# Optimization experiments

Hardware: AMD Instinct MI355X
Metric: run time of the kernel (lower is better)

## Reference

```python
import math
import jax, jax.numpy as jnp
import numpy as np

OLEN = 512
RATIO = 0.5
DROP_P = 0.2


def _gat(x, src, dst, W, a_s, a_d, b):
    """PyG GATConv (heads=1, concat=True, add_self_loops=True, neg_slope=0.2)."""
    n = x.shape[0]
    loops = jnp.arange(n, dtype=src.dtype)
    s = jnp.concatenate([src, loops])  # [E+N] source nodes
    d = jnp.concatenate([dst, loops])  # [E+N] destination nodes
    h = x @ W                           # [N, H]
    alpha_s = h @ a_s                   # [N]
    alpha_d = h @ a_d                   # [N]
    e = jax.nn.leaky_relu(alpha_s[s] + alpha_d[d], 0.2)  # [E+N]
    # segment softmax over destination neighborhoods
    m = jax.ops.segment_max(e, d, num_segments=n)
    ee = jnp.exp(e - m[d])
    denom = jax.ops.segment_sum(ee, d, num_segments=n)
    alpha = ee / denom[d]
    out = jax.ops.segment_sum(alpha[:, None] * h[s], d, num_segments=n)
    return out + b


def _forward(x, src, dst, W1, a_src1, a_dst1, b1, W2, a_src2, a_dst2, b2,
             W3, a_src3, a_dst3, b3, W_rel, W_root, b_pool):
    N, E = x.shape[0], src.shape[0]
    key = jax.random.key(42)
    h = x
    for i, (W, a_s, a_d, b) in enumerate([(W1, a_src1, a_dst1, b1),
                                          (W2, a_src2, a_dst2, b2),
                                          (W3, a_src3, a_dst3, b3)]):
        h = jax.nn.relu(_gat(h, src, dst, W, a_s, a_d, b))
        keep = jax.random.bernoulli(jax.random.fold_in(key, i), 1.0 - DROP_P, h.shape)
        h = jnp.where(keep, h / (1.0 - DROP_P), 0.0)  # F.dropout(training=True)

    # SAGPooling(GraphConv score, ratio=0.5, tanh) repeated until n <= 512.
    # Node counts are static per iteration (k = ceil(0.5*n)); edge arrays keep
    # fixed size E with a validity mask (edges dropped when an endpoint is pooled away).
    cur_src, cur_dst = src, dst
    emask = jnp.ones((E,), dtype=h.dtype)
    n = N
    while True:
        agg = jax.ops.segment_sum(h[cur_src] * emask[:, None], cur_dst, num_segments=n)
        score = (agg @ W_rel + h @ W_root + b_pool)[:, 0]  # GraphConv(d->1), aggr='add'
        score = jnp.tanh(score)
        k = math.ceil(RATIO * n)
        top_vals, perm = jax.lax.top_k(score, k)
        h = h[perm] * top_vals[:, None]
        inv = jnp.full((n,), -1, dtype=cur_src.dtype).at[perm].set(
            jnp.arange(k, dtype=cur_src.dtype))
        ns, nd = inv[cur_src], inv[cur_dst]
        valid = (ns >= 0) & (nd >= 0)
        emask = emask * valid.astype(emask.dtype)
        cur_src = jnp.where(valid, ns, 0)
        cur_dst = jnp.where(valid, nd, 0)
        n = k
        if n <= OLEN:
            break

    out = jnp.zeros((OLEN, h.shape[1]), h.dtype).at[:n].set(h)
    return out


def setup_inputs() -> dict:
    key = jax.random.key(0)
    ks = jax.random.split(key, 20)
    N, E, IDIM, HDIM = 50000, 800000, 128, 200
    inp = {
        "x": jax.random.normal(ks[0], (N, IDIM), jnp.float32),
        "src": jax.random.randint(ks[1], (E,), 0, N, jnp.int32),
        "dst": jax.random.randint(ks[2], (E,), 0, N, jnp.int32),
    }
    def w(k, shape, fan_in):
        return jax.random.normal(k, shape, jnp.float32) / np.sqrt(fan_in).astype(np.float32)
    inp["W1"] = w(ks[3], (IDIM, HDIM), IDIM)
    inp["a_src1"] = w(ks[4], (HDIM,), HDIM)
    inp["a_dst1"] = w(ks[5], (HDIM,), HDIM)
    inp["b1"] = jnp.zeros((HDIM,), jnp.float32)
    inp["W2"] = w(ks[6], (HDIM, HDIM), HDIM)
    inp["a_src2"] = w(ks[7], (HDIM,), HDIM)
    inp["a_dst2"] = w(ks[8], (HDIM,), HDIM)
    inp["b2"] = jnp.zeros((HDIM,), jnp.float32)
    inp["W3"] = w(ks[9], (HDIM, HDIM), HDIM)
    inp["a_src3"] = w(ks[10], (HDIM,), HDIM)
    inp["a_dst3"] = w(ks[11], (HDIM,), HDIM)
    inp["b3"] = jnp.zeros((HDIM,), jnp.float32)
    inp["W_rel"] = w(ks[12], (HDIM, 1), HDIM)
    inp["W_root"] = w(ks[13], (HDIM, 1), HDIM)
    inp["b_pool"] = jnp.zeros((1,), jnp.float32)
    return inp


def reference(x, src, dst, W1, a_src1, a_dst1, b1, W2, a_src2, a_dst2, b2,
              W3, a_src3, a_dst3, b3, W_rel, W_root, b_pool):
    return _forward(x, src, dst, W1, a_src1, a_dst1, b1, W2, a_src2, a_dst2, b2,
                    W3, a_src3, a_dst3, b3, W_rel, W_root, b_pool)
```

## Files before the change

kernel.cpp:

```cpp
#include <hip/hip_runtime.h>
#include <cstdint>
#include <cstddef>


__host__ __device__ inline void tf_round(uint32_t &x0, uint32_t &x1, int r) {
  x0 += x1;
  x1 = (x1 << r) | (x1 >> (32 - r));
  x1 ^= x0;
}

__host__ __device__ inline void threefry2x32(uint32_t k0, uint32_t k1,
                                             uint32_t &x0, uint32_t &x1) {
  uint32_t ks2 = k0 ^ k1 ^ 0x1BD11BDAu;
  x0 += k0; x1 += k1;
  tf_round(x0, x1, 13); tf_round(x0, x1, 15); tf_round(x0, x1, 26); tf_round(x0, x1, 6);
  x0 += k1; x1 += ks2 + 1u;
  tf_round(x0, x1, 17); tf_round(x0, x1, 29); tf_round(x0, x1, 16); tf_round(x0, x1, 24);
  x0 += ks2; x1 += k0 + 2u;
  tf_round(x0, x1, 13); tf_round(x0, x1, 15); tf_round(x0, x1, 26); tf_round(x0, x1, 6);
  x0 += k0; x1 += k1 + 3u;
  tf_round(x0, x1, 17); tf_round(x0, x1, 29); tf_round(x0, x1, 16); tf_round(x0, x1, 24);
  x0 += k1; x1 += ks2 + 4u;
  tf_round(x0, x1, 13); tf_round(x0, x1, 15); tf_round(x0, x1, 26); tf_round(x0, x1, 6);
  x0 += ks2; x1 += k0 + 5u;
}

__global__ __launch_bounds__(256) void gemm200_k(
    const float* __restrict__ A, const float* __restrict__ B,
    float* __restrict__ C, int M, int K) {
  __shared__ float As[128 * 9];
  __shared__ __align__(16) float Bs[8][208];
  int tid = threadIdx.x;
  int m0 = blockIdx.x * 128;
  int r = tid >> 2;
  int colBase = (tid & 3) * 52;
  int nq = (colBase == 156) ? 11 : 13;
  float acc0[52], acc1[52];
#pragma unroll
  for (int q = 0; q < 52; q++) { acc0[q] = 0.f; acc1[q] = 0.f; }

  int arow = tid >> 1;
  int ac = (tid & 1) * 4;
  int gmA = m0 + arow;
  const float* Aptr = A + (size_t)gmA * K + ac;
  int bk0 = tid / 50, bc0 = (tid - bk0 * 50) * 4;
  int t2 = tid + 256;
  int bk1 = t2 / 50, bc1 = (t2 - bk1 * 50) * 4;
  bool hasB1 = (t2 < 400);

  float4 va = make_float4(0.f, 0.f, 0.f, 0.f);
  if (gmA < M) va = *(const float4*)(Aptr);
  float4 vb0 = *(const float4*)(B + (size_t)bk0 * 200 + bc0);
  float4 vb1 = make_float4(0.f, 0.f, 0.f, 0.f);
  if (hasB1) vb1 = *(const float4*)(B + (size_t)bk1 * 200 + bc1);

  for (int k0 = 0; k0 < K; k0 += 8) {
    As[arow * 9 + ac + 0] = va.x;
    As[arow * 9 + ac + 1] = va.y;
    As[arow * 9 + ac + 2] = va.z;
    As[arow * 9 + ac + 3] = va.w;
    *(float4*)(&Bs[bk0][bc0]) = vb0;
    if (hasB1) *(float4*)(&Bs[bk1][bc1]) = vb1;
    __syncthreads();
    int kn = k0 + 8;
    if (kn < K) {
      if (gmA < M) va = *(const float4*)(Aptr + kn);
      vb0 = *(const float4*)(B + (size_t)(kn + bk0) * 200 + bc0);
      if (hasB1) vb1 = *(const float4*)(B + (size_t)(kn + bk1) * 200 + bc1);
    }
#pragma unroll
    for (int kk = 0; kk < 8; kk++) {
      float a0 = As[r * 9 + kk];
      float a1 = As[(r + 64) * 9 + kk];
#pragma unroll
      for (int q = 0; q < 13; q++) {
        float4 b = *(const float4*)(&Bs[kk][colBase + 4 * q]);
        acc0[4 * q + 0] += a0 * b.x; acc0[4 * q + 1] += a0 * b.y;
        acc0[4 * q + 2] += a0 * b.z; acc0[4 * q + 3] += a0 * b.w;
        acc1[4 * q + 0] += a1 * b.x; acc1[4 * q + 1] += a1 * b.y;
        acc1[4 * q + 2] += a1 * b.z; acc1[4 * q + 3] += a1 * b.w;
      }
    }
    __syncthreads();
  }
  int gm0 = m0 + r, gm1 = m0 + r + 64;
#pragma unroll
  for (int q = 0; q < 13; q++) {
    if (q < nq) {
      int col = colBase + 4 * q;
      float4 v0 = make_float4(acc0[4 * q + 0], acc0[4 * q + 1],
                              acc0[4 * q + 2], acc0[4 * q + 3]);
      float4 v1 = make_float4(acc1[4 * q + 0], acc1[4 * q + 1],
                              acc1[4 * q + 2], acc1[4 * q + 3]);
      if (gm0 < M) *(float4*)(C + (size_t)gm0 * 200 + col) = v0;
      if (gm1 < M) *(float4*)(C + (size_t)gm1 * 200 + col) = v1;
    }
  }
}

__global__ __launch_bounds__(256) void dual_dot_k(
    const float* __restrict__ H, const float* __restrict__ v1,
    const float* __restrict__ v2, float* __restrict__ o1,
    float* __restrict__ o2, int n) {
  int wave = blockIdx.x * 4 + (threadIdx.x >> 6);
  int lane = threadIdx.x & 63;
  if (wave >= n) return;
  const float* row = H + (size_t)wave * 200;
  float s1 = 0.f, s2 = 0.f;
  for (int d = lane; d < 200; d += 64) {
    float h = row[d];
    s1 += h * v1[d];
    s2 += h * v2[d];
  }
  for (int off = 32; off; off >>= 1) {
    s1 += __shfl_down(s1, off);
    s2 += __shfl_down(s2, off);
  }
  if (lane == 0) { o1[wave] = s1; o2[wave] = s2; }
}

__global__ __launch_bounds__(256) void indeg_k(const int* __restrict__ dst,
                                               int* __restrict__ cnt, int E) {
  int e = blockIdx.x * 256 + threadIdx.x;
  if (e < E) atomicAdd(&cnt[dst[e]], 1);
}

__global__ __launch_bounds__(256) void scan_k(const int* __restrict__ cnt,
                                              int* __restrict__ rowptr, int N) {
  __shared__ int psum[256];
  int t = threadIdx.x;
  int CH = (N + 255) / 256;
  int beg = t * CH, end = min(beg + CH, N);
  if (beg > N) { beg = N; }
  int s = 0;
  for (int i = beg; i < end; i++) s += cnt[i];
  psum[t] = s;
  __syncthreads();
  if (t == 0) {
    int run = 0;
    for (int i = 0; i < 256; i++) { int v = psum[i]; psum[i] = run; run += v; }
  }
  __syncthreads();
  int run = psum[t];
  for (int i = beg; i < end; i++) { rowptr[i] = run; run += cnt[i]; }
  if (end == N && beg <= N) rowptr[N] = run;
}

__global__ __launch_bounds__(256) void cpyint_k(const int* __restrict__ a,
                                                int* __restrict__ b, int n) {
  int i = blockIdx.x * 256 + threadIdx.x;
  if (i < n) b[i] = a[i];
}

__global__ __launch_bounds__(256) void place_k(const int* __restrict__ dst,
                                               int* __restrict__ curs,
                                               int* __restrict__ csr, int E) {
  int e = blockIdx.x * 256 + threadIdx.x;
  if (e >= E) return;
  int pos = atomicAdd(&curs[dst[e]], 1);
  csr[pos] = e;
}

__global__ __launch_bounds__(256) void sortrow_k(const int* __restrict__ rowptr,
                                                 int* __restrict__ csr, int N) {
  int d = blockIdx.x * 256 + threadIdx.x;
  if (d >= N) return;
  int b = rowptr[d], e2 = rowptr[d + 1];
  for (int i = b + 1; i < e2; i++) {
    int v = csr[i];
    int j = i - 1;
    while (j >= b && csr[j] > v) { csr[j + 1] = csr[j]; j--; }
    csr[j + 1] = v;
  }
}

__device__ inline float dec_ord(unsigned enc) {
  unsigned b = (enc & 0x80000000u) ? (enc ^ 0x80000000u) : ~enc;
  return __uint_as_float(b);
}

__global__ __launch_bounds__(256) void edge_max_k(
    const int* __restrict__ src, const int* __restrict__ dst,
    const float* __restrict__ as_, const float* __restrict__ ad_,
    unsigned* __restrict__ menc, int E, int N) {
  int j = blockIdx.x * 256 + threadIdx.x;
  if (j >= E + N) return;
  int s, d;
  if (j < E) { s = src[j]; d = dst[j]; } else { s = j - E; d = s; }
  float v = as_[s] + ad_[d];
  float ev = (v >= 0.f) ? v : 0.2f * v;
  unsigned b = __float_as_uint(ev);
  unsigned enc = (b & 0x80000000u) ? ~b : (b | 0x80000000u);
  atomicMax(&menc[d], enc);
}

__global__ __launch_bounds__(256) void eeden_k(
    const int* __restrict__ rowptr, const int* __restrict__ csr,
    const int* __restrict__ src, const float* __restrict__ as_,
    const float* __restrict__ ad_, const unsigned* __restrict__ menc,
    int2* __restrict__ pk, float* __restrict__ eeS, float* __restrict__ den,
    int N) {
  int d = blockIdx.x * 256 + threadIdx.x;
  if (d >= N) return;
  float m = dec_ord(menc[d]);
  float adv = ad_[d];
  int b = rowptr[d], e2 = rowptr[d + 1];
  float s = 0.f;
  for (int i = b; i < e2; i++) {
    int e = csr[i];
    int sv = src[e];
    float v = as_[sv] + adv;
    float ev = (v >= 0.f) ? v : 0.2f * v;
    float ee = expf(ev - m);
    pk[i] = make_int2(sv, __float_as_int(ee));
    s = __fadd_rn(s, ee);
  }
  float vS = as_[d] + adv;
  float evS = (vS >= 0.f) ? vS : 0.2f * vS;
  float eS = expf(evS - m);
  eeS[d] = eS;
  s = __fadd_rn(s, eS);
  den[d] = s;
}

#define GLD(s) (*(const float4*)(Hl + (size_t)(s) * 200))
#define ACC(W_, H_)                                    \
  acc.x = __fadd_rn(acc.x, __fmul_rn((W_), (H_).x));   \
  acc.y = __fadd_rn(acc.y, __fmul_rn((W_), (H_).y));   \
  acc.z = __fadd_rn(acc.z, __fmul_rn((W_), (H_).z));   \
  acc.w = __fadd_rn(acc.w, __fmul_rn((W_), (H_).w));

__global__ __launch_bounds__(256) void gat_out_k(
    const int* __restrict__ rowptr, const int2* __restrict__ pk,
    const float* __restrict__ eeS, const float* __restrict__ den,
    const float* __restrict__ HW, float* __restrict__ OUT, int N) {
  int node = blockIdx.x * 4 + (threadIdx.x >> 6);
  int lane = threadIdx.x & 63;
  if (node >= N || lane >= 50) return;
  int b = rowptr[node];
  int deg = rowptr[node + 1] - b;
  int cnt = deg + 1;
  float dn = den[node];
  const float* __restrict__ Hl = HW + 4 * lane;

  auto fS = [&](int t, int &s, float &w) {
    if (t < deg) {
      int2 p = pk[b + t];
      s = p.x;
      w = __fdiv_rn(__int_as_float(p.y), dn);
    } else if (t == deg) {
      s = node;
      w = __fdiv_rn(eeS[node], dn);
    } else {
      s = node;
      w = 0.f;
    }
  };

  int sa, sb, sc, sd, se, sf, sn;
  float w0, w1, w2, w3, w4, w5, wn;
  fS(0, sa, w0); fS(1, sb, w1); fS(2, sc, w2); fS(3, sd, w3);
  float4 h0 = GLD(sa), h1 = GLD(sb), h2 = GLD(sc), h3 = GLD(sd);
  fS(4, se, w4);
  fS(5, sf, w5);

  float4 acc = make_float4(0.f, 0.f, 0.f, 0.f);
  for (int t = 0; t < cnt; t++) {
    float4 h4 = GLD(se);
    fS(t + 6, sn, wn);
    ACC(w0, h0);
    h0 = h1; h1 = h2; h2 = h3; h3 = h4;
    w0 = w1; w1 = w2; w2 = w3; w3 = w4; w4 = w5; w5 = wn;
    se = sf; sf = sn;
  }
  *(float4*)(OUT + (size_t)node * 200 + 4 * lane) = acc;
}

__global__ __launch_bounds__(256) void epi_k(float* __restrict__ H,
                                             const float* __restrict__ bias,
                                             uint32_t k0, uint32_t k1, int total) {
  int t = blockIdx.x * 256 + threadIdx.x;
  if (t >= total) return;
  uint32_t x0 = 0u, x1 = (uint32_t)t;
  threefry2x32(k0, k1, x0, x1);
  uint32_t bits = x0 ^ x1;
  float u = __uint_as_float((bits >> 9) | 0x3f800000u) - 1.0f;
  int col = t % 200;
  float v = H[t] + bias[col];
  v = fmaxf(v, 0.f);
  H[t] = (u < 0.8f) ? (v / 0.8f) : 0.f;
}

__global__ __launch_bounds__(256) void einit_k(
    const int* __restrict__ src, const int* __restrict__ dst,
    int* __restrict__ cs, int* __restrict__ cd, int* __restrict__ orig,
    int E, int N) {
  int e = blockIdx.x * 256 + threadIdx.x;
  if (e < E) { cs[e] = src[e]; cd[e] = dst[e]; }
  if (e < N) orig[e] = e;
}

__global__ __launch_bounds__(256) void pool_agg_k(
    const int* __restrict__ rowptr, const int* __restrict__ csr,
    const int* __restrict__ csrc, const int* __restrict__ orig,
    const float* __restrict__ H, const float* __restrict__ wrel,
    const float* __restrict__ wroot, const float* __restrict__ bp,
    float* __restrict__ score, int n) {
  __shared__ float sagg[4][200];
  int wv = threadIdx.x >> 6;
  int node = blockIdx.x * 4 + wv;
  int lane = threadIdx.x & 63;
  if (node >= n) return;
  int o = orig[node];
  int b = rowptr[o];
  int deg = rowptr[o + 1] - b;

  if (lane < 50) {
    const float* __restrict__ Hl = H + 4 * lane;
    auto fS = [&](int t, int &s, float &w) {
      if (t < deg) {
        int e = csr[b + t];
        int sv = csrc[e];
        s = (sv >= 0) ? sv : 0;
        w = (sv >= 0) ? 1.f : 0.f;
      } else {
        s = 0;
        w = 0.f;
      }
    };

    int sa, sb, sc, sd, se, sf, sn;
    float w0, w1, w2, w3, w4, w5, wn;
    fS(0, sa, w0); fS(1, sb, w1); fS(2, sc, w2); fS(3, sd, w3);
    float4 h0 = GLD(sa), h1 = GLD(sb), h2 = GLD(sc), h3 = GLD(sd);
    fS(4, se, w4);
    fS(5, sf, w5);

    float4 acc = make_float4(0.f, 0.f, 0.f, 0.f);
    for (int t = 0; t < deg; t++) {
      float4 h4 = GLD(se);
      fS(t + 6, sn, wn);
      ACC(w0, h0);
      h0 = h1; h1 = h2; h2 = h3; h3 = h4;
      w0 = w1; w1 = w2; w2 = w3; w3 = w4; w4 = w5; w5 = wn;
      se = sf; sf = sn;
    }
    sagg[wv][4 * lane + 0] = acc.x;
    sagg[wv][4 * lane + 1] = acc.y;
    sagg[wv][4 * lane + 2] = acc.z;
    sagg[wv][4 * lane + 3] = acc.w;
  }
  __threadfence_block();

  const float* arow = sagg[wv];
  const float* hrow = H + (size_t)node * 200;
  float s1 = 0.f, s2 = 0.f;
  for (int d = lane; d < 200; d += 64) {
    s1 += arow[d] * wrel[d];
    s2 += hrow[d] * wroot[d];
  }
  for (int off = 32; off; off >>= 1) {
    s1 += __shfl_down(s1, off);
    s2 += __shfl_down(s2, off);
  }
  if (lane == 0) score[node] = tanhf((s1 + s2) + bp[0]);
}
#undef GLD
#undef ACC


__global__ __launch_bounds__(256) void rhenc_k(const float* __restrict__ score,
                                               unsigned* __restrict__ keyA,
                                               int* __restrict__ payA,
                                               int* __restrict__ counts,
                                               int n, int NB) {
  __shared__ int hist[256];
  hist[threadIdx.x] = 0;
  __syncthreads();
  int i = blockIdx.x * 256 + threadIdx.x;
  if (i < n) {
    unsigned b = __float_as_uint(score[i]);
    if (b == 0x80000000u) b = 0u;
    unsigned enc = (b & 0x80000000u) ? ~b : (b | 0x80000000u);
    unsigned key = ~enc;
    keyA[i] = key;
    payA[i] = i;
    atomicAdd(&hist[key & 255u], 1);
  }
  __syncthreads();
  counts[threadIdx.x * NB + blockIdx.x] = hist[threadIdx.x];
}

__global__ __launch_bounds__(256) void rscan_k(int* __restrict__ counts,
                                               int* __restrict__ base, int NB) {
  __shared__ int tot[256];
  int t = threadIdx.x;
  int s = 0;
  for (int b = 0; b < NB; b++) s += counts[t * NB + b];
  tot[t] = s;
  __syncthreads();
  if (t == 0) {
    int run = 0;
    for (int i = 0; i < 256; i++) { int v = tot[i]; tot[i] = run; run += v; }
  }
  __syncthreads();
  int run = tot[t];
  for (int b = 0; b < NB; b++) {
    int c = counts[t * NB + b];
    base[t * NB + b] = run;
    run += c;
    counts[t * NB + b] = 0;
  }
}

__global__ __launch_bounds__(256) void rscatter_k(
    const unsigned* __restrict__ keyIn, const int* __restrict__ payIn,
    const int* __restrict__ base, unsigned* __restrict__ keyOut,
    int* __restrict__ payOut, int* __restrict__ countsNext,
    int n, int NB, int shift) {
  __shared__ int dig[256];
  int t = threadIdx.x;
  int i = blockIdx.x * 256 + t;
  unsigned k = 0u;
  int p = 0, d = -1;
  if (i < n) {
    k = keyIn[i];
    p = payIn[i];
    d = (int)((k >> shift) & 255u);
  }
  dig[t] = d;
  __syncthreads();
  if (i < n) {
    int local = 0;
    for (int j = 0; j < t; j++) local += (dig[j] == d) ? 1 : 0;
    int pos = base[d * NB + blockIdx.x] + local;
    keyOut[pos] = k;
    payOut[pos] = p;
    int nd = (int)((k >> (shift + 8)) & 255u);
    atomicAdd(&countsNext[nd * NB + (pos >> 8)], 1);
  }
}

__global__ __launch_bounds__(256) void rscatterF_k(
    const unsigned* __restrict__ keyIn, const int* __restrict__ payIn,
    const int* __restrict__ base, const int* __restrict__ oin,
    int* __restrict__ oout, int* __restrict__ perm, int* __restrict__ inv,
    int n, int NB, int k) {
  __shared__ int dig[256];
  int t = threadIdx.x;
  int i = blockIdx.x * 256 + t;
  int p = 0, d = -1;
  if (i < n) {
    p = payIn[i];
    d = (int)((keyIn[i] >> 24) & 255u);
  }
  dig[t] = d;
  __syncthreads();
  if (i < n) {
    int local = 0;
    for (int j = 0; j < t; j++) local += (dig[j] == d) ? 1 : 0;
    int pos = base[d * NB + blockIdx.x] + local;
    if (pos < k) { perm[pos] = p; inv[p] = pos; oout[pos] = oin[p]; }
    else inv[p] = -1;
  }
}

__global__ __launch_bounds__(256) void gather_k(
    const float* __restrict__ H, const int* __restrict__ perm,
    const float* __restrict__ score, float* __restrict__ Ho, int k) {
  int r = blockIdx.x;
  int d = threadIdx.x;
  int p = perm[r];
  float s = score[p];
  if (d < 200) Ho[(size_t)r * 200 + d] = __fmul_rn(H[(size_t)p * 200 + d], s);
}

__global__ __launch_bounds__(256) void remap_k(int* __restrict__ cs,
                                               int* __restrict__ cd,
                                               const int* __restrict__ inv, int E) {
  int e = blockIdx.x * 256 + threadIdx.x;
  if (e >= E) return;
  int a = cs[e];
  if (a < 0) return;
  int na = inv[a], nb = inv[cd[e]];
  bool valid = (na >= 0) && (nb >= 0);
  cs[e] = valid ? na : -1;
  cd[e] = valid ? nb : -1;
}

__global__ __launch_bounds__(256) void out_copy_k(const float* __restrict__ h,
                                                  float* __restrict__ out, int cnt) {
  int t = blockIdx.x * 256 + threadIdx.x;
  if (t < cnt) out[t] = h[t];
}

extern "C" void kernel_launch(void* const* d_in, const int* in_sizes, int n_in,
                              void* d_out, int out_size, void* d_ws, size_t ws_size,
                              hipStream_t stream) {
  const int ID = 128, HD = 200;
  const int N = in_sizes[0] / ID;
  const int E = in_sizes[1];
  const int ET = E + N;
  const int total = N * HD;

  const float* x = (const float*)d_in[0];
  const int* src = (const int*)d_in[1];
  const int* dst = (const int*)d_in[2];
  const float* W[3]   = {(const float*)d_in[3], (const float*)d_in[7], (const float*)d_in[11]};
  const float* asv[3] = {(const float*)d_in[4], (const float*)d_in[8], (const float*)d_in[12]};
  const float* adv[3] = {(const float*)d_in[5], (const float*)d_in[9], (const float*)d_in[13]};
  const float* bv[3]  = {(const float*)d_in[6], (const float*)d_in[10], (const float*)d_in[14]};
  const float* Wrel  = (const float*)d_in[15];
  const float* Wroot = (const float*)d_in[16];
  const float* bpool = (const float*)d_in[17];

  char* ws = (char*)d_ws;
  float*    bufA  = (float*)(ws + 0);
  float*    bufB  = (float*)(ws + 40000000);
  float*    as_   = (float*)(ws + 80000000);
  float*    ad_   = (float*)(ws + 80200000);
  float*    ee_   = (float*)(ws + 80400000);
  unsigned* menc  = (unsigned*)(ws + 83800000);
  float*    den   = (float*)(ws + 84000000);
  float*    score = (float*)(ws + 84200000);
  int*      rank_ = (int*)(ws + 84400000);
  int*      perm_ = (int*)(ws + 84600000);
  int*      inv_  = (int*)(ws + 84800000);
  int*      origA = (int*)(ws + 85000000);
  int*      origB = (int*)(ws + 85200000);
  int*      rowptr= (int*)(ws + 85400000);
  int*      curs  = (int*)(ws + 85650000);
  int*      csr   = (int*)(ws + 85850000);
  int*      csrc  = (int*)(ws + 89050000);
  int*      cdst  = (int*)(ws + 92250000);

  int2* pk = (int2*)(ws + 89050000);
  float* eeS = (float*)(ws + 80400000);

  char* rx = ws + 80400000;
  unsigned* keyA   = (unsigned*)(rx + 0 * 262144);
  unsigned* keyB   = (unsigned*)(rx + 1 * 262144);
  int*      payA   = (int*)(rx + 2 * 262144);
  int*      payB   = (int*)(rx + 3 * 262144);
  int*      rcounts= (int*)(rx + 4 * 262144);
  int*      rbase  = (int*)(rx + 5 * 262144);

  uint32_t fk0[3], fk1[3];
  for (int i = 0; i < 3; i++) {
    uint32_t a = 0u, b = (uint32_t)i;
    threefry2x32(0u, 42u, a, b);
    fk0[i] = a; fk1[i] = b;
  }

  const int B256 = 256;
  hipMemsetAsync(rank_, 0, (size_t)N * 4, stream);
  indeg_k<<<(E + 255) / 256, B256, 0, stream>>>(dst, rank_, E);
  scan_k<<<1, B256, 0, stream>>>(rank_, rowptr, N);
  cpyint_k<<<(N + 255) / 256, B256, 0, stream>>>(rowptr, curs, N);
  place_k<<<(E + 255) / 256, B256, 0, stream>>>(dst, curs, csr, E);
  sortrow_k<<<(N + 255) / 256, B256, 0, stream>>>(rowptr, csr, N);

  for (int i = 0; i < 3; i++) {
    const float* in = (i == 0) ? x : bufB;
    int K = (i == 0) ? ID : HD;
    gemm200_k<<<(N + 127) / 128, B256, 0, stream>>>(in, W[i], bufA, N, K);
    dual_dot_k<<<(N + 3) / 4, B256, 0, stream>>>(bufA, asv[i], adv[i], as_, ad_, N);
    hipMemsetAsync(menc, 0, (size_t)N * 4, stream);
    edge_max_k<<<(ET + 255) / 256, B256, 0, stream>>>(src, dst, as_, ad_, menc, E, N);
    eeden_k<<<(N + 255) / 256, B256, 0, stream>>>(rowptr, csr, src, as_, ad_, menc,
                                                  pk, eeS, den, N);
    gat_out_k<<<(N + 3) / 4, B256, 0, stream>>>(rowptr, pk, eeS, den, bufA, bufB, N);
    epi_k<<<(total + 255) / 256, B256, 0, stream>>>(bufB, bv[i], fk0[i], fk1[i], total);
  }

  einit_k<<<(E + 255) / 256, B256, 0, stream>>>(src, dst, csrc, cdst, origA, E, N);
  float* hcur = bufB;
  float* hnext = bufA;
  int* ocur = origA;
  int* onext = origB;
  int n = N;
  while (true) {
    int k = (n + 1) / 2;
    int NB = (n + 255) / 256;
    pool_agg_k<<<(n + 3) / 4, B256, 0, stream>>>(rowptr, csr, csrc, ocur, hcur,
                                                 Wrel, Wroot, bpool, score, n);
    rhenc_k<<<NB, B256, 0, stream>>>(score, keyA, payA, rcounts, n, NB);
    rscan_k<<<1, B256, 0, stream>>>(rcounts, rbase, NB);
    rscatter_k<<<NB, B256, 0, stream>>>(keyA, payA, rbase, keyB, payB, rcounts, n, NB, 0);
    rscan_k<<<1, B256, 0, stream>>>(rcounts, rbase, NB);
    rscatter_k<<<NB, B256, 0, stream>>>(keyB, payB, rbase, keyA, payA, rcounts, n, NB, 8);
    rscan_k<<<1, B256, 0, stream>>>(rcounts, rbase, NB);
    rscatter_k<<<NB, B256, 0, stream>>>(keyA, payA, rbase, keyB, payB, rcounts, n, NB, 16);
    rscan_k<<<1, B256, 0, stream>>>(rcounts, rbase, NB);
    rscatterF_k<<<NB, B256, 0, stream>>>(keyB, payB, rbase, ocur, onext, perm_, inv_,
                                         n, NB, k);
    gather_k<<<k, B256, 0, stream>>>(hcur, perm_, score, hnext, k);
    remap_k<<<(E + 255) / 256, B256, 0, stream>>>(csrc, cdst, inv_, E);
    { float* t = hcur; hcur = hnext; hnext = t; }
    { int* t = ocur; ocur = onext; onext = t; }
    n = k;
    if (n <= 512) break;
  }

  hipMemsetAsync(d_out, 0, (size_t)out_size * 4, stream);
  out_copy_k<<<(n * HD + 255) / 256, B256, 0, stream>>>(hcur, (float*)d_out, n * HD);
}
```

Baseline: 2.843 ms.

## Fuse segment max into eeden, epilogue into gat_out, single-block radix sort for small n

New measurement: 3.287 ms. 1.16x slower.

```diff
diff --git a/kernel.cpp b/kernel.cpp
--- a/kernel.cpp
+++ b/kernel.cpp
@@ -179,36 +179,36 @@
   return __uint_as_float(b);
 }
 
-__global__ __launch_bounds__(256) void edge_max_k(
-    const int* __restrict__ src, const int* __restrict__ dst,
-    const float* __restrict__ as_, const float* __restrict__ ad_,
-    unsigned* __restrict__ menc, int E, int N) {
-  int j = blockIdx.x * 256 + threadIdx.x;
-  if (j >= E + N) return;
-  int s, d;
-  if (j < E) { s = src[j]; d = dst[j]; } else { s = j - E; d = s; }
-  float v = as_[s] + ad_[d];
-  float ev = (v >= 0.f) ? v : 0.2f * v;
+__device__ inline unsigned enc_ord(float ev) {
   unsigned b = __float_as_uint(ev);
-  unsigned enc = (b & 0x80000000u) ? ~b : (b | 0x80000000u);
-  atomicMax(&menc[d], enc);
+  return (b & 0x80000000u) ? ~b : (b | 0x80000000u);
 }
 
 __global__ __launch_bounds__(256) void eeden_k(
     const int* __restrict__ rowptr, const int* __restrict__ csr,
     const int* __restrict__ src, const float* __restrict__ as_,
-    const float* __restrict__ ad_, const unsigned* __restrict__ menc,
-    int2* __restrict__ pk, float* __restrict__ eeS, float* __restrict__ den,
-    int N) {
+    const float* __restrict__ ad_, int2* __restrict__ pk,
+    float* __restrict__ eeS, float* __restrict__ den, int N) {
   int d = blockIdx.x * 256 + threadIdx.x;
   if (d >= N) return;
-  float m = dec_ord(menc[d]);
   float adv = ad_[d];
   int b = rowptr[d], e2 = rowptr[d + 1];
+  unsigned mx = 0u;
+  for (int i = b; i < e2; i++) {
+    int sv = src[csr[i]];
+    float v = as_[sv] + adv;
+    float ev = (v >= 0.f) ? v : 0.2f * v;
+    mx = max(mx, enc_ord(ev));
+  }
+  {
+    float v = as_[d] + adv;
+    float ev = (v >= 0.f) ? v : 0.2f * v;
+    mx = max(mx, enc_ord(ev));
+  }
+  float m = dec_ord(mx);
   float s = 0.f;
   for (int i = b; i < e2; i++) {
-    int e = csr[i];
-    int sv = src[e];
+    int sv = src[csr[i]];
     float v = as_[sv] + adv;
     float ev = (v >= 0.f) ? v : 0.2f * v;
     float ee = expf(ev - m);
@@ -233,7 +233,8 @@
 __global__ __launch_bounds__(256) void gat_out_k(
     const int* __restrict__ rowptr, const int2* __restrict__ pk,
     const float* __restrict__ eeS, const float* __restrict__ den,
-    const float* __restrict__ HW, float* __restrict__ OUT, int N) {
+    const float* __restrict__ HW, const float* __restrict__ bias,
+    float* __restrict__ OUT, uint32_t tk0, uint32_t tk1, int N) {
   int node = blockIdx.x * 4 + (threadIdx.x >> 6);
   int lane = threadIdx.x & 63;
   if (node >= N || lane >= 50) return;
@@ -273,22 +274,24 @@
     w0 = w1; w1 = w2; w2 = w3; w3 = w4; w4 = w5; w5 = wn;
     se = sf; sf = sn;
   }
-  *(float4*)(OUT + (size_t)node * 200 + 4 * lane) = acc;
-}
-
-__global__ __launch_bounds__(256) void epi_k(float* __restrict__ H,
-                                             const float* __restrict__ bias,
-                                             uint32_t k0, uint32_t k1, int total) {
-  int t = blockIdx.x * 256 + threadIdx.x;
-  if (t >= total) return;
-  uint32_t x0 = 0u, x1 = (uint32_t)t;
-  threefry2x32(k0, k1, x0, x1);
-  uint32_t bits = x0 ^ x1;
-  float u = __uint_as_float((bits >> 9) | 0x3f800000u) - 1.0f;
-  int col = t % 200;
-  float v = H[t] + bias[col];
-  v = fmaxf(v, 0.f);
-  H[t] = (u < 0.8f) ? (v / 0.8f) : 0.f;
+
+  float4 bv4 = *(const float4*)(bias + 4 * lane);
+  float vin[4] = {acc.x, acc.y, acc.z, acc.w};
+  float bb4[4] = {bv4.x, bv4.y, bv4.z, bv4.w};
+  float vout[4];
+  int tbase = node * 200 + 4 * lane;
+#pragma unroll
+  for (int j = 0; j < 4; j++) {
+    uint32_t x0 = 0u, x1 = (uint32_t)(tbase + j);
+    threefry2x32(tk0, tk1, x0, x1);
+    uint32_t bits = x0 ^ x1;
+    float u = __uint_as_float((bits >> 9) | 0x3f800000u) - 1.0f;
+    float v = vin[j] + bb4[j];
+    v = fmaxf(v, 0.f);
+    vout[j] = (u < 0.8f) ? (v / 0.8f) : 0.f;
+  }
+  *(float4*)(OUT + (size_t)node * 200 + 4 * lane) =
+      make_float4(vout[0], vout[1], vout[2], vout[3]);
 }
 
 __global__ __launch_bounds__(256) void einit_k(
@@ -381,8 +384,7 @@
   if (i < n) {
     unsigned b = __float_as_uint(score[i]);
     if (b == 0x80000000u) b = 0u;
-    unsigned enc = (b & 0x80000000u) ? ~b : (b | 0x80000000u);
-    unsigned key = ~enc;
+    unsigned key = ~enc_ord(__uint_as_float(b));
     keyA[i] = key;
     payA[i] = i;
     atomicAdd(&hist[key & 255u], 1);
@@ -465,6 +467,69 @@
   }
 }
 
+__global__ __launch_bounds__(256) void rsmall_k(
+    const float* __restrict__ score, const int* __restrict__ oin,
+    int* __restrict__ oout, int* __restrict__ perm, int* __restrict__ inv,
+    unsigned* __restrict__ keyA, unsigned* __restrict__ keyB,
+    int* __restrict__ payA, int* __restrict__ payB, int n, int kk) {
+  __shared__ int hist[256];
+  __shared__ int basev[256];
+  __shared__ int dig[256];
+  int t = threadIdx.x;
+  for (int i = t; i < n; i += 256) {
+    unsigned b = __float_as_uint(score[i]);
+    if (b == 0x80000000u) b = 0u;
+    keyA[i] = ~enc_ord(__uint_as_float(b));
+    payA[i] = i;
+  }
+  __syncthreads();
+  unsigned* ki = keyA; unsigned* ko = keyB;
+  int* pi = payA; int* po = payB;
+  for (int pass = 0; pass < 4; pass++) {
+    int shift = pass * 8;
+    hist[t] = 0;
+    __syncthreads();
+    for (int i = t; i < n; i += 256)
+      atomicAdd(&hist[(ki[i] >> shift) & 255u], 1);
+    __syncthreads();
+    if (t == 0) {
+      int run = 0;
+      for (int i = 0; i < 256; i++) { int v = hist[i]; basev[i] = run; run += v; }
+    }
+    __syncthreads();
+    int nch = (n + 255) / 256;
+    for (int c = 0; c < nch; c++) {
+      int i = c * 256 + t;
+      unsigned kv = 0u;
+      int pv = 0, d = -1;
+      if (i < n) { kv = ki[i]; pv = pi[i]; d = (int)((kv >> shift) & 255u); }
+      dig[t] = d;
+      __syncthreads();
+      if (i < n) {
+        int local = 0;
+        for (int j = 0; j < t; j++) local += (dig[j] == d) ? 1 : 0;
+        int pos = basev[d] + local;
+        if (pass < 3) {
+          ko[pos] = kv;
+          po[pos] = pv;
+        } else {
+          if (pos < kk) { perm[pos] = pv; inv[pv] = pos; oout[pos] = oin[pv]; }
+          else inv[pv] = -1;
+        }
+      }
+      __syncthreads();
+      hist[t] = 0;
+      __syncthreads();
+      if (i < n) atomicAdd(&hist[d], 1);
+      __syncthreads();
+      basev[t] += hist[t];
+      __syncthreads();
+    }
+    unsigned* tk = ki; ki = ko; ko = tk;
+    int* tp = pi; pi = po; po = tp;
+  }
+}
+
 __global__ __launch_bounds__(256) void gather_k(
     const float* __restrict__ H, const int* __restrict__ perm,
     const float* __restrict__ score, float* __restrict__ Ho, int k) {
@@ -500,7 +565,6 @@
   const int ID = 128, HD = 200;
   const int N = in_sizes[0] / ID;
   const int E = in_sizes[1];
-  const int ET = E + N;
   const int total = N * HD;
 
   const float* x = (const float*)d_in[0];
@@ -519,8 +583,6 @@
   float*    bufB  = (float*)(ws + 40000000);
   float*    as_   = (float*)(ws + 80000000);
   float*    ad_   = (float*)(ws + 80200000);
-  float*    ee_   = (float*)(ws + 80400000);
-  unsigned* menc  = (unsigned*)(ws + 83800000);
   float*    den   = (float*)(ws + 84000000);
   float*    score = (float*)(ws + 84200000);
   int*      rank_ = (int*)(ws + 84400000);
@@ -565,12 +627,10 @@
     int K = (i == 0) ? ID : HD;
     gemm200_k<<<(N + 127) / 128, B256, 0, stream>>>(in, W[i], bufA, N, K);
     dual_dot_k<<<(N + 3) / 4, B256, 0, stream>>>(bufA, asv[i], adv[i], as_, ad_, N);
-    hipMemsetAsync(menc, 0, (size_t)N * 4, stream);
-    edge_max_k<<<(ET + 255) / 256, B256, 0, stream>>>(src, dst, as_, ad_, menc, E, N);
-    eeden_k<<<(N + 255) / 256, B256, 0, stream>>>(rowptr, csr, src, as_, ad_, menc,
+    eeden_k<<<(N + 255) / 256, B256, 0, stream>>>(rowptr, csr, src, as_, ad_,
                                                   pk, eeS, den, N);
-    gat_out_k<<<(N + 3) / 4, B256, 0, stream>>>(rowptr, pk, eeS, den, bufA, bufB, N);
-    epi_k<<<(total + 255) / 256, B256, 0, stream>>>(bufB, bv[i], fk0[i], fk1[i], total);
+    gat_out_k<<<(N + 3) / 4, B256, 0, stream>>>(rowptr, pk, eeS, den, bufA,
+                                                bv[i], bufB, fk0[i], fk1[i], N);
   }
 
   einit_k<<<(E + 255) / 256, B256, 0, stream>>>(src, dst, csrc, cdst, origA, E, N);
@@ -584,16 +644,21 @@
     int NB = (n + 255) / 256;
     pool_agg_k<<<(n + 3) / 4, B256, 0, stream>>>(rowptr, csr, csrc, ocur, hcur,
                                                  Wrel, Wroot, bpool, score, n);
-    rhenc_k<<<NB, B256, 0, stream>>>(score, keyA, payA, rcounts, n, NB);
-    rscan_k<<<1, B256, 0, stream>>>(rcounts, rbase, NB);
-    rscatter_k<<<NB, B256, 0, stream>>>(keyA, payA, rbase, keyB, payB, rcounts, n, NB, 0);
-    rscan_k<<<1, B256, 0, stream>>>(rcounts, rbase, NB);
-    rscatter_k<<<NB, B256, 0, stream>>>(keyB, payB, rbase, keyA, payA, rcounts, n, NB, 8);
-    rscan_k<<<1, B256, 0, stream>>>(rcounts, rbase, NB);
-    rscatter_k<<<NB, B256, 0, stream>>>(keyA, payA, rbase, keyB, payB, rcounts, n, NB, 16);
-    rscan_k<<<1, B256, 0, stream>>>(rcounts, rbase, NB);
-    rscatterF_k<<<NB, B256, 0, stream>>>(keyB, payB, rbase, ocur, onext, perm_, inv_,
-                                         n, NB, k);
+    if (n <= 4096) {
+      rsmall_k<<<1, B256, 0, stream>>>(score, ocur, onext, perm_, inv_,
+                                       keyA, keyB, payA, payB, n, k);
+    } else {
+      rhenc_k<<<NB, B256, 0, stream>>>(score, keyA, payA, rcounts, n, NB);
+      rscan_k<<<1, B256, 0, stream>>>(rcounts, rbase, NB);
+      rscatter_k<<<NB, B256, 0, stream>>>(keyA, payA, rbase, keyB, payB, rcounts, n, NB, 0);
+      rscan_k<<<1, B256, 0, stream>>>(rcounts, rbase, NB);
+      rscatter_k<<<NB, B256, 0, stream>>>(keyB, payB, rbase, keyA, payA, rcounts, n, NB, 8);
+      rscan_k<<<1, B256, 0, stream>>>(rcounts, rbase, NB);
+      rscatter_k<<<NB, B256, 0, stream>>>(keyA, payA, rbase, keyB, payB, rcounts, n, NB, 16);
+      rscan_k<<<1, B256, 0, stream>>>(rcounts, rbase, NB);
+      rscatterF_k<<<NB, B256, 0, stream>>>(keyB, payB, rbase, ocur, onext, perm_, inv_,
+                                           n, NB, k);
+    }
     gather_k<<<k, B256, 0, stream>>>(hcur, perm_, score, hnext, k);
     remap_k<<<(E + 255) / 256, B256, 0, stream>>>(csrc, cdst, inv_, E);
     { float* t = hcur; hcur = hnext; hnext = t; }
```
